# Kernel tuning notes

Measured on AMD Instinct MI355X. Metric: run time of the kernel, lower is better.

Reference implementation:

```python
import jax, jax.numpy as jnp
import numpy as np


def setup_inputs() -> dict:
    key = jax.random.key(0)
    ks = jax.random.split(key, 5)
    B, Cin, Cout, H, W, L, K = 16, 512, 512, 64, 64, 512, 3
    return {
        "content": jax.random.normal(ks[0], (B, Cin, H, W), jnp.float32),
        "latent": jax.random.normal(ks[1], (B, L), jnp.float32),
        "noise": jax.random.normal(ks[2], (B, 1, H, W), jnp.float32),
        "affine_w": jax.random.normal(ks[3], (Cin, L), jnp.float32),
        "affine_b": jnp.ones((Cin,), jnp.float32),  # ConvLayer fills affine bias with 1
        "conv_w": jax.random.normal(ks[4], (Cout, Cin, K, K), jnp.float32),
        "bias": jnp.zeros((1, Cout, 1, 1), jnp.float32),
        "noise_weight": jnp.asarray(0.1, jnp.float32),  # nonzero so noise path is exercised
    }


def reference(content, latent, noise, affine_w, affine_b, conv_w, bias, noise_weight):
    L = affine_w.shape[1]
    # affine (LinearLayer, lrelu=False): weight scaled by sqrt(1/inChannels), lrMultiplier=1
    style = latent @ (affine_w * np.sqrt(1.0 / L)).T + affine_b  # [B, Cin]
    # modulate: per-sample weights [B, Cout, Cin, k, k]
    w = conv_w[None] * style[:, None, :, None, None]
    # demodulate
    norm = jax.lax.rsqrt(jnp.sum(jnp.square(w), axis=(2, 3, 4), keepdims=True) + 1e-8)
    w = w * norm
    pad = conv_w.shape[-1] // 2
    # groups=batch trick == per-sample conv; vmap over batch
    def conv1(x, wk):  # x: [Cin,H,W], wk: [Cout,Cin,k,k]
        return jax.lax.conv_general_dilated(x[None], wk, (1, 1), [(pad, pad), (pad, pad)])[0]
    out = jax.vmap(conv1)(content, w)  # [B, Cout, H, W]
    out = out + noise_weight * noise
    out = jax.nn.leaky_relu(out + bias, negative_slope=0.2) * np.sqrt(2.0)
    return out
```

## Files before the change

kernel.cpp:

```cpp
#include <hip/hip_runtime.h>
#include <hip/hip_bf16.h>


typedef float f32x4 __attribute__((ext_vector_type(4)));
typedef short bf16x8 __attribute__((ext_vector_type(8)));
typedef int i32x4 __attribute__((ext_vector_type(4)));

#define BB 16
#define CIN 512
#define COUT 512
#define HH 64
#define WW 64
#define LL 512

#define XS_OFF 0
#define XS_SZ (BB * HH * WW * CIN * 2)
#define WT_OFF (XS_OFF + XS_SZ)
#define WT_SZ (9 * COUT * CIN * 2)
#define STYLE_OFF (WT_OFF + WT_SZ)
#define STYLE_SZ (BB * CIN * 4)
#define WSQ_OFF (STYLE_OFF + STYLE_SZ)
#define WSQ_SZ (COUT * CIN * 4)
#define DEM_OFF (WSQ_OFF + WSQ_SZ)
#define DEM_SZ (BB * COUT * 4)
#define WS_NEEDED (DEM_OFF + DEM_SZ)

#define XS_STRIDE 66
#define XROWB (XS_STRIDE * 64)
#define XROWS 6
#define XSZ (XROWS * XROWB)
#define WTAPB (64 * 64)
#define WSZ (9 * WTAPB)
#define LDSZ (XSZ + WSZ)

__device__ __forceinline__ void gld_lds16(const void* g, void* l) {
  __builtin_amdgcn_global_load_lds(
      (const __attribute__((address_space(1))) unsigned int*)g,
      (__attribute__((address_space(3))) unsigned int*)l, 16, 0, 0);
}

__global__ void style_kernel(const float* __restrict__ latent,
                             const float* __restrict__ affine_w,
                             const float* __restrict__ affine_b,
                             float* __restrict__ style) {
  const int idx = blockIdx.x * 256 + threadIdx.x;
  const int b = idx >> 9, ci = idx & 511;
  const float* lp = latent + b * LL;
  const float* wp = affine_w + ci * LL;
  float acc = 0.f;
  for (int l = 0; l < LL; ++l) acc += lp[l] * wp[l];
  style[idx] = acc * 0.044194173824159216f + affine_b[ci];
}

__global__ void wprep_kernel(const float* __restrict__ conv_w,
                             float* __restrict__ wsq,
                             __hip_bfloat16* __restrict__ wt) {
  const int idx = blockIdx.x * 256 + threadIdx.x;
  const int co = idx >> 9, ci = idx & 511;
  const float* wp = conv_w + idx * 9;
  float ss = 0.f;
#pragma unroll
  for (int t = 0; t < 9; ++t) {
    float v = wp[t];
    ss += v * v;
    wt[(t * COUT + co) * CIN + ci] = __float2bfloat16(v);
  }
  wsq[idx] = ss;
}

__global__ void dem_kernel(const float* __restrict__ wsq,
                           const float* __restrict__ style,
                           float* __restrict__ dem) {
  const int idx = blockIdx.x * 256 + threadIdx.x;
  const int b = idx >> 9, co = idx & 511;
  const float* sp = style + b * CIN;
  const float* wp = wsq + co * CIN;
  float acc = 0.f;
  for (int ci = 0; ci < CIN; ++ci) {
    float s = sp[ci];
    acc += wp[ci] * s * s;
  }
  dem[idx] = 1.0f / sqrtf(acc + 1e-8f);
}

__global__ void xsprep_kernel(const float* __restrict__ content,
                              const float* __restrict__ style,
                              __hip_bfloat16* __restrict__ xs) {
  __shared__ float tile[64][65];
  const int b = blockIdx.x >> 6;
  const int y = blockIdx.x & 63;
  const int tid = threadIdx.x;
  for (int cb = 0; cb < 8; ++cb) {
    const int ci0 = cb * 64;
    {
      const int x = tid & 63;
      const int c0 = tid >> 6;
#pragma unroll
      for (int p = 0; p < 16; ++p) {
        const int ci = p * 4 + c0;
        tile[ci][x] = content[((b * CIN + ci0 + ci) * HH + y) * WW + x];
      }
    }
    __syncthreads();
    {
      const int ci = tid & 63;
      const int x0 = tid >> 6;
      const float st = style[b * CIN + ci0 + ci];
#pragma unroll
      for (int p = 0; p < 16; ++p) {
        const int x = p * 4 + x0;
        xs[((b * HH + y) * WW + x) * CIN + ci0 + ci] =
            __float2bfloat16(tile[ci][x] * st);
      }
    }
    __syncthreads();
  }
}

__global__ __launch_bounds__(256, 2) void conv_kernel(
    const __hip_bfloat16* __restrict__ xs,
    const __hip_bfloat16* __restrict__ wt,
    const float* __restrict__ dem,
    const float* __restrict__ noise,
    const float* __restrict__ biasp,
    const float* __restrict__ nwp,
    float* __restrict__ out) {
  __shared__ __attribute__((aligned(16))) char lds[LDSZ];

  const int tid = threadIdx.x;
  const int lane = tid & 63;
  const int wv = tid >> 6;
  const int bid = blockIdx.x;
  const int cot = bid & 7;
  const int yq = (bid >> 3) & 15;
  const int b = bid >> 7;
  const int co0 = cot << 6;
  const int y0 = yq << 2;

  for (int off = tid * 16; off < XSZ; off += 256 * 16)
    *(i32x4*)(lds + off) = (i32x4){0, 0, 0, 0};

  const int l15 = lane & 15;
  const int kg = lane >> 4;

  int aoff[4];
#pragma unroll
  for (int mf = 0; mf < 4; ++mf) {
    const int co_l = l15 + mf * 16;
    const int fs = (co_l & 3) ^ ((co_l >> 2) & 3);
    aoff[mf] = co_l * 64 + ((kg ^ fs) << 4);
  }
  int boff[4][3];
#pragma unroll
  for (int nf = 0; nf < 4; ++nf)
#pragma unroll
    for (int dx = 0; dx < 3; ++dx) {
      const int s = nf * 16 + l15 + dx;
      const int fs = (s & 3) ^ ((s >> 2) & 3);
      boff[nf][dx] = s * 64 + ((kg ^ fs) << 4);
    }

  const int rlo = (yq == 0) ? 1 : 0;
  const int rhi = (yq == 15) ? 4 : 5;
  const int nxc = (rhi - rlo + 1) * 4;
  const int ntot = nxc + 36;

  const int xsub = lane >> 2;
  const int slotl = lane & 3;

  f32x4 acc[4][4];
#pragma unroll
  for (int mf = 0; mf < 4; ++mf)
#pragma unroll
    for (int nf = 0; nf < 4; ++nf) acc[mf][nf] = (f32x4){0.f, 0.f, 0.f, 0.f};

  __syncthreads();

  for (int cib = 0; cib < 16; ++cib) {
    const int ci0 = cib * 32;
    for (int c = wv; c < ntot; c += 4) {
      if (c < nxc) {
        const int r = rlo + (c >> 2);
        const int q = c & 3;
        const int s = 1 + q * 16 + xsub;
        const int x = s - 1;
        const int y = y0 + r - 1;
        const int dcig = slotl ^ ((s & 3) ^ ((s >> 2) & 3));
        const __hip_bfloat16* g =
            xs + (((b << 6) + y) << 6 | x) * CIN + ci0 + dcig * 8;
        gld_lds16(g, lds + r * XROWB + 64 + q * 1024);
      } else {
        const int cw = c - nxc;
        const int tap = cw >> 2;
        const int q = cw & 3;
        const int co = q * 16 + xsub;
        const int dcig = slotl ^ ((co & 3) ^ ((co >> 2) & 3));
        const __hip_bfloat16* g =
            wt + ((tap << 9) + co0 + co) * CIN + ci0 + dcig * 8;
        gld_lds16(g, lds + XSZ + tap * WTAPB + q * 1024);
      }
    }
    __syncthreads();

#pragma unroll
    for (int dy = 0; dy < 3; ++dy) {
      const int rbase = (wv + dy) * XROWB;
#pragma unroll
      for (int dx = 0; dx < 3; ++dx) {
        const int tap = dy * 3 + dx;
        bf16x8 a[4];
#pragma unroll
        for (int mf = 0; mf < 4; ++mf)
          a[mf] = *(const bf16x8*)(lds + XSZ + tap * WTAPB + aoff[mf]);
#pragma unroll
        for (int nf = 0; nf < 4; ++nf) {
          const bf16x8 bfr = *(const bf16x8*)(lds + rbase + boff[nf][dx]);
#pragma unroll
          for (int mf = 0; mf < 4; ++mf)
            acc[mf][nf] = __builtin_amdgcn_mfma_f32_16x16x32_bf16(
                a[mf], bfr, acc[mf][nf], 0, 0, 0);
        }
      }
    }
    __syncthreads();
  }

  const float nwv = nwp[0];
  const int y = y0 + wv;
  float nz[4];
#pragma unroll
  for (int nf = 0; nf < 4; ++nf)
    nz[nf] = nwv * noise[(b << 12) + (y << 6) + nf * 16 + l15];

#pragma unroll
  for (int mf = 0; mf < 4; ++mf) {
    const int cobase = co0 + mf * 16 + kg * 4;
    const f32x4 dm = *(const f32x4*)(dem + (b << 9) + cobase);
    const f32x4 bs = *(const f32x4*)(biasp + cobase);
#pragma unroll
    for (int r2 = 0; r2 < 4; ++r2) {
      const int co = cobase + r2;
      float* op = out + ((((b << 9) + co) << 12) | (y << 6) | l15);
      const float d = dm[r2];
      const float bsv = bs[r2];
#pragma unroll
      for (int nf = 0; nf < 4; ++nf) {
        float v = acc[mf][nf][r2] * d + nz[nf] + bsv;
        v = (v > 0.f ? v : 0.2f * v) * 1.41421356237309515f;
        op[nf * 16] = v;
      }
    }
  }
}

extern "C" void kernel_launch(void* const* d_in, const int* in_sizes, int n_in,
                              void* d_out, int out_size, void* d_ws, size_t ws_size,
                              hipStream_t stream) {
  const float* content  = (const float*)d_in[0];
  const float* latent   = (const float*)d_in[1];
  const float* noise    = (const float*)d_in[2];
  const float* affine_w = (const float*)d_in[3];
  const float* affine_b = (const float*)d_in[4];
  const float* conv_w   = (const float*)d_in[5];
  const float* bias     = (const float*)d_in[6];
  const float* nw       = (const float*)d_in[7];
  float* out = (float*)d_out;
  char* ws = (char*)d_ws;

  if (ws_size < (size_t)WS_NEEDED) return;

  __hip_bfloat16* xs = (__hip_bfloat16*)(ws + XS_OFF);
  __hip_bfloat16* wt = (__hip_bfloat16*)(ws + WT_OFF);
  float* style = (float*)(ws + STYLE_OFF);
  float* wsq   = (float*)(ws + WSQ_OFF);
  float* dem   = (float*)(ws + DEM_OFF);

  style_kernel<<<dim3(32), dim3(256), 0, stream>>>(latent, affine_w, affine_b, style);
  wprep_kernel<<<dim3(1024), dim3(256), 0, stream>>>(conv_w, wsq, wt);
  dem_kernel<<<dim3(32), dim3(256), 0, stream>>>(wsq, style, dem);
  xsprep_kernel<<<dim3(1024), dim3(256), 0, stream>>>(content, style, xs);
  conv_kernel<<<dim3(2048), dim3(256), 0, stream>>>(xs, wt, dem, noise, bias, nw, out);
}
```

Before: 348.0 us.

## Enlarge conv tile to eight output rows per block and reuse weight fragments across rows

Each block now computes 8 output rows (two per wave) instead of 4, halving the grid to 1024 blocks. Weight fragments for all three dy taps are loaded once per dx and reused across input rows, which cuts weight LDS and global traffic per output. Block indices are remapped so consecutive dispatches spread across XCDs. The costs are double the accumulator registers, a larger LDS input tile, and possibly lower occupancy and fewer blocks to balance across CUs.

```diff
diff --git a/kernel.cpp b/kernel.cpp
--- a/kernel.cpp
+++ b/kernel.cpp
@@ -27,7 +27,7 @@
 
 #define XS_STRIDE 66
 #define XROWB (XS_STRIDE * 64)
-#define XROWS 6
+#define XROWS 10
 #define XSZ (XROWS * XROWB)
 #define WTAPB (64 * 64)
 #define WSZ (9 * WTAPB)
@@ -130,12 +130,14 @@
   const int tid = threadIdx.x;
   const int lane = tid & 63;
   const int wv = tid >> 6;
-  const int bid = blockIdx.x;
-  const int cot = bid & 7;
-  const int yq = (bid >> 3) & 15;
-  const int b = bid >> 7;
+
+  const int d = blockIdx.x;
+  const int L = (d & 7) * 128 + (d >> 3);
+  const int cot = L & 7;
+  const int yo = (L >> 3) & 7;
+  const int b = L >> 6;
   const int co0 = cot << 6;
-  const int y0 = yq << 2;
+  const int y0 = yo << 3;
 
   for (int off = tid * 16; off < XSZ; off += 256 * 16)
     *(i32x4*)(lds + off) = (i32x4){0, 0, 0, 0};
@@ -152,27 +154,27 @@
   }
   int boff[4][3];
 #pragma unroll
-  for (int nf = 0; nf < 4; ++nf)
+  for (int q = 0; q < 4; ++q)
 #pragma unroll
     for (int dx = 0; dx < 3; ++dx) {
-      const int s = nf * 16 + l15 + dx;
+      const int s = q * 16 + l15 + dx;
       const int fs = (s & 3) ^ ((s >> 2) & 3);
-      boff[nf][dx] = s * 64 + ((kg ^ fs) << 4);
-    }
-
-  const int rlo = (yq == 0) ? 1 : 0;
-  const int rhi = (yq == 15) ? 4 : 5;
+      boff[q][dx] = s * 64 + ((kg ^ fs) << 4);
+    }
+
+  const int rlo = (yo == 0) ? 1 : 0;
+  const int rhi = (yo == 7) ? 8 : 9;
   const int nxc = (rhi - rlo + 1) * 4;
   const int ntot = nxc + 36;
 
   const int xsub = lane >> 2;
   const int slotl = lane & 3;
 
-  f32x4 acc[4][4];
+  f32x4 acc[4][8];
 #pragma unroll
   for (int mf = 0; mf < 4; ++mf)
 #pragma unroll
-    for (int nf = 0; nf < 4; ++nf) acc[mf][nf] = (f32x4){0.f, 0.f, 0.f, 0.f};
+    for (int nf = 0; nf < 8; ++nf) acc[mf][nf] = (f32x4){0.f, 0.f, 0.f, 0.f};
 
   __syncthreads();
 
@@ -202,23 +204,34 @@
     }
     __syncthreads();
 
-#pragma unroll
-    for (int dy = 0; dy < 3; ++dy) {
-      const int rbase = (wv + dy) * XROWB;
-#pragma unroll
-      for (int dx = 0; dx < 3; ++dx) {
-        const int tap = dy * 3 + dx;
-        bf16x8 a[4];
+    const int rowbase = (2 * wv) * XROWB;
+#pragma unroll
+    for (int dx = 0; dx < 3; ++dx) {
+      bf16x8 a[3][4];
+#pragma unroll
+      for (int dy = 0; dy < 3; ++dy)
 #pragma unroll
         for (int mf = 0; mf < 4; ++mf)
-          a[mf] = *(const bf16x8*)(lds + XSZ + tap * WTAPB + aoff[mf]);
-#pragma unroll
-        for (int nf = 0; nf < 4; ++nf) {
-          const bf16x8 bfr = *(const bf16x8*)(lds + rbase + boff[nf][dx]);
-#pragma unroll
-          for (int mf = 0; mf < 4; ++mf)
-            acc[mf][nf] = __builtin_amdgcn_mfma_f32_16x16x32_bf16(
-                a[mf], bfr, acc[mf][nf], 0, 0, 0);
+          a[dy][mf] =
+              *(const bf16x8*)(lds + XSZ + (dy * 3 + dx) * WTAPB + aoff[mf]);
+#pragma unroll
+      for (int ir = 0; ir < 4; ++ir) {
+        const char* rp = lds + rowbase + ir * XROWB;
+        bf16x8 bq[4];
+#pragma unroll
+        for (int q = 0; q < 4; ++q)
+          bq[q] = *(const bf16x8*)(rp + boff[q][dx]);
+#pragma unroll
+        for (int dy = 0; dy < 3; ++dy) {
+          const int r = ir - dy;
+          if (r == 0 || r == 1) {
+#pragma unroll
+            for (int q = 0; q < 4; ++q)
+#pragma unroll
+              for (int mf = 0; mf < 4; ++mf)
+                acc[mf][r * 4 + q] = __builtin_amdgcn_mfma_f32_16x16x32_bf16(
+                    a[dy][mf], bq[q], acc[mf][r * 4 + q], 0, 0, 0);
+          }
         }
       }
     }
@@ -226,28 +239,31 @@
   }
 
   const float nwv = nwp[0];
-  const int y = y0 + wv;
-  float nz[4];
-#pragma unroll
-  for (int nf = 0; nf < 4; ++nf)
-    nz[nf] = nwv * noise[(b << 12) + (y << 6) + nf * 16 + l15];
-
-#pragma unroll
-  for (int mf = 0; mf < 4; ++mf) {
-    const int cobase = co0 + mf * 16 + kg * 4;
-    const f32x4 dm = *(const f32x4*)(dem + (b << 9) + cobase);
-    const f32x4 bs = *(const f32x4*)(biasp + cobase);
-#pragma unroll
-    for (int r2 = 0; r2 < 4; ++r2) {
-      const int co = cobase + r2;
-      float* op = out + ((((b << 9) + co) << 12) | (y << 6) | l15);
-      const float d = dm[r2];
-      const float bsv = bs[r2];
-#pragma unroll
-      for (int nf = 0; nf < 4; ++nf) {
-        float v = acc[mf][nf][r2] * d + nz[nf] + bsv;
-        v = (v > 0.f ? v : 0.2f * v) * 1.41421356237309515f;
-        op[nf * 16] = v;
+#pragma unroll
+  for (int r = 0; r < 2; ++r) {
+    const int y = y0 + 2 * wv + r;
+    float nz[4];
+#pragma unroll
+    for (int q = 0; q < 4; ++q)
+      nz[q] = nwv * noise[(b << 12) + (y << 6) + q * 16 + l15];
+
+#pragma unroll
+    for (int mf = 0; mf < 4; ++mf) {
+      const int cobase = co0 + mf * 16 + kg * 4;
+      const f32x4 dm = *(const f32x4*)(dem + (b << 9) + cobase);
+      const f32x4 bs = *(const f32x4*)(biasp + cobase);
+#pragma unroll
+      for (int r2 = 0; r2 < 4; ++r2) {
+        const int co = cobase + r2;
+        float* op = out + ((((b << 9) + co) << 12) | (y << 6) | l15);
+        const float dmv = dm[r2];
+        const float bsv = bs[r2];
+#pragma unroll
+        for (int q = 0; q < 4; ++q) {
+          float v = acc[mf][r * 4 + q][r2] * dmv + nz[q] + bsv;
+          v = (v > 0.f ? v : 0.2f * v) * 1.41421356237309515f;
+          op[q * 16] = v;
+        }
       }
     }
   }
@@ -279,5 +295,5 @@
   wprep_kernel<<<dim3(1024), dim3(256), 0, stream>>>(conv_w, wsq, wt);
   dem_kernel<<<dim3(32), dim3(256), 0, stream>>>(wsq, style, dem);
   xsprep_kernel<<<dim3(1024), dim3(256), 0, stream>>>(content, style, xs);
-  conv_kernel<<<dim3(2048), dim3(256), 0, stream>>>(xs, wt, dem, noise, bias, nw, out);
-}
+  conv_kernel<<<dim3(1024), dim3(256), 0, stream>>>(xs, wt, dem, noise, bias, nw, out);
+}
```

New measurement: 313.2 us. -10.0%, faster.
